# Kernel tuning notes

Hardware: AMD Instinct MI355X
Metric: run time of the kernel (lower is better)

The kernel has to match this reference:

```python
import jax, jax.numpy as jnp
import numpy as np

B, S, E = 2, 2048, 2048
HQ, HKV, D = 16, 4, 128
WINDOW = 512
ROPE_BASE = 10000.0


def apply_rope(x):
    # x: [B, H, S, D]; rotate-half RoPE, positions start at 0 (prefill, no cache)
    half = x.shape[-1] // 2
    inv_freq = 1.0 / (ROPE_BASE ** (jnp.arange(half, dtype=jnp.float32) / half))
    ang = jnp.arange(x.shape[2], dtype=jnp.float32)[:, None] * inv_freq[None, :]  # [S, half]
    cos, sin = jnp.cos(ang), jnp.sin(ang)
    x1, x2 = x[..., :half], x[..., half:]
    return jnp.concatenate([x1 * cos - x2 * sin, x1 * sin + x2 * cos], axis=-1)


def setup_inputs() -> dict:
    key = jax.random.key(0)
    ks = jax.random.split(key, 9)
    sc = 0.02
    return {
        "x": jax.random.normal(ks[0], (B, S, E), dtype=jnp.float32),
        "Wq": jax.random.normal(ks[1], (HQ * D, E), dtype=jnp.float32) * sc,
        "bq": jnp.zeros((HQ * D,), dtype=jnp.float32),
        "Wk": jax.random.normal(ks[2], (HKV * D, E), dtype=jnp.float32) * sc,
        "bk": jnp.zeros((HKV * D,), dtype=jnp.float32),
        "Wv": jax.random.normal(ks[3], (HKV * D, E), dtype=jnp.float32) * sc,
        "bv": jnp.zeros((HKV * D,), dtype=jnp.float32),
        "Wo": jax.random.normal(ks[4], (E, HQ * D), dtype=jnp.float32) * sc,
        "bo": jnp.zeros((E,), dtype=jnp.float32),
    }


def reference(x, Wq, bq, Wk, bk, Wv, bv, Wo, bo):
    b, s, _ = x.shape
    group = HQ // HKV
    # projections (torch Linear: y = x @ W.T + b)
    Q = (x @ Wq.T + bq).reshape(b, s, HQ, D).transpose(0, 2, 1, 3)     # [B,HQ,S,D]
    K = (x @ Wk.T + bk).reshape(b, s, HKV, D).transpose(0, 2, 1, 3)    # [B,HKV,S,D]
    V = (x @ Wv.T + bv).reshape(b, s, HKV, D).transpose(0, 2, 1, 3)
    Q = apply_rope(Q)
    K = apply_rope(K)
    # GQA: group query heads per KV head instead of repeating K/V (same math)
    Qg = Q.reshape(b, HKV, group, s, D)
    scores = jnp.einsum('bkgqd,bkyd->bkgqy', Qg, K) / jnp.sqrt(jnp.float32(D))
    # sliding-window causal mask: j <= i and i - j <= window_size
    i = jnp.arange(s)[:, None]
    j = jnp.arange(s)[None, :]
    allowed = (j <= i) & ((i - j) <= WINDOW)
    scores = jnp.where(allowed, scores, jnp.float32(-jnp.inf))
    w = jax.nn.softmax(scores, axis=-1)
    out = jnp.einsum('bkgqy,bkyd->bkgqd', w, V)                        # [B,HKV,G,S,D]
    out = out.reshape(b, HQ, s, D).transpose(0, 2, 1, 3).reshape(b, s, HQ * D)
    out = out @ Wo.T + bo  # dropout is identity at inference
    return out
```

## Files before the change

kernel.cpp:

```cpp
#include <hip/hip_runtime.h>
#include <hip/hip_bf16.h>

typedef unsigned short u16;
typedef unsigned int u32;
typedef __attribute__((ext_vector_type(4))) unsigned short ushort4_t;
typedef __attribute__((ext_vector_type(8))) short short8;
typedef __attribute__((ext_vector_type(4))) float f32x4;

#define B_ 2
#define S_ 2048
#define E_ 2048
#define HQ_ 16
#define HKV_ 4
#define D_ 128
#define WINDOW_ 512

static __device__ __forceinline__ float bf2f(u16 u) {
    union { unsigned int i; float f; } v; v.i = ((unsigned int)u) << 16; return v.f;
}
static __device__ __forceinline__ u16 f2bf(float f) {
    unsigned int x = __float_as_uint(f);
    unsigned int r = (x + 0x7fffu + ((x >> 16) & 1u)) >> 16;
    return (u16)r;
}

static __device__ __forceinline__ void gload_lds16(const u16* g, u16* l) {
    __builtin_amdgcn_global_load_lds(
        (const __attribute__((address_space(1))) unsigned int*)g,
        (__attribute__((address_space(3))) unsigned int*)l,
        16, 0, 0);
}

static __device__ __forceinline__ int detect_fp32(const u16* wq, int* cnt_sh) {
    if (threadIdx.x == 0) *cnt_sh = 0;
    __syncthreads();
    int c = 0;
    #pragma unroll
    for (int k = 0; k < 4; ++k) {
        u16 v = wq[threadIdx.x * 4 + k];
        if (((v >> 7) & 0xFF) >= 0x90) c++;
    }
    atomicAdd(cnt_sh, c);
    __syncthreads();
    return (*cnt_sh >= 64) ? 1 : 0;
}

#define C_WQ   8388608u
#define C_WK   12582912u
#define C_WV   13631488u
#define C_BQ   14680064u
#define C_BK   14682112u
#define C_BV   14682624u
#define C_WO   14683136u
#define C_BO   18877440u
#define NTOT   18879488u

__global__ __launch_bounds__(256) void convert_kernel(
    const void* p0, const void* p1, const void* p2, const void* p3, const void* p4,
    const void* p5, const void* p6, const void* p7, const void* p8,
    u16* __restrict__ C, int* __restrict__ flagout)
{
    __shared__ int cnt;
    const int f = detect_fp32((const u16*)p1, &cnt);
    if (blockIdx.x == 0 && threadIdx.x == 0) *flagout = f;

    unsigned int idx = (blockIdx.x * 256u + threadIdx.x) * 4u;
    if (idx >= NTOT) return;

    const void* src; unsigned int local;
    if      (idx < C_WQ) { src = p0; local = idx; }
    else if (idx < C_WK) { src = p1; local = idx - C_WQ; }
    else if (idx < C_WV) { src = p3; local = idx - C_WK; }
    else if (idx < C_BQ) { src = p5; local = idx - C_WV; }
    else if (idx < C_BK) { src = p2; local = idx - C_BQ; }
    else if (idx < C_BV) { src = p4; local = idx - C_BK; }
    else if (idx < C_WO) { src = p6; local = idx - C_BV; }
    else if (idx < C_BO) { src = p7; local = idx - C_WO; }
    else                 { src = p8; local = idx - C_BO; }

    ushort4_t o;
    if (f) {
        float4 v = *(const float4*)((const float*)src + local);
        o[0] = f2bf(v.x); o[1] = f2bf(v.y); o[2] = f2bf(v.z); o[3] = f2bf(v.w);
    } else {
        o = *(const ushort4_t*)((const u16*)src + local);
    }
    *(ushort4_t*)(C + idx) = o;
}

#define SCHED __builtin_amdgcn_sched_barrier(0)

__global__ __launch_bounds__(512, 2) void gemm256(
    const u16* __restrict__ A, const u16* __restrict__ W,
    const u16* __restrict__ bias, u16* __restrict__ C,
    int M, int N, int K)
{
    __shared__ __align__(16) u16 lds[65536];

    const int m0 = blockIdx.y * 256, n0 = blockIdx.x * 256;
    const int t = threadIdx.x;
    const int wv = t >> 6, lane = t & 63;
    const int wm = wv >> 2, wn = wv & 3;
    const int quad = lane >> 4, l16 = lane & 15;
    const int h3 = l16 & 7;

    const int rr = t >> 3;
    const int sblk = ((t & 7) ^ (rr & 7)) * 8;

    const u16* Asrc = A + (size_t)(m0 + rr) * K + sblk;
    const u16* Bsrc = W + (size_t)(n0 + rr) * K + sblk;
    u16* ldsA = lds + wv * 512;
    u16* ldsB = lds + 16384 + wv * 512;

#define STAGE_A(slot, Qi, k0) gload_lds16(Asrc + (size_t)((Qi) * 64) * K + (k0), ldsA + (slot) * 32768 + (Qi) * 4096)
#define STAGE_B(slot, Qi, k0) gload_lds16(Bsrc + (size_t)((Qi) * 64) * K + (k0), ldsB + (slot) * 32768 + (Qi) * 4096)

    f32x4 acc[8][4];
    #pragma unroll
    for (int mi = 0; mi < 8; ++mi)
        #pragma unroll
        for (int ni = 0; ni < 4; ++ni)
            acc[mi][ni] = (f32x4){0.f, 0.f, 0.f, 0.f};

    const int NT = K / 64;

    #pragma unroll
    for (int q = 0; q < 4; ++q) STAGE_A(0, q, 0);
    #pragma unroll
    for (int q = 0; q < 4; ++q) STAGE_B(0, q, 0);
    SCHED;
    STAGE_A(1, 0, 64);
    STAGE_A(1, 2, 64);
    SCHED;
    asm volatile("s_waitcnt vmcnt(2)" ::: "memory");
    __builtin_amdgcn_s_barrier();
    SCHED;

    short8 aA[4][2], aB[4][2];
    short8 b0[2][2], b1[2][2];

#define DSREAD_A(dst, qm_)                                                     \
    _Pragma("unroll")                                                          \
    for (int fr = 0; fr < 4; ++fr) {                                           \
        const int r = wm * 128 + (qm_) * 64 + fr * 16 + l16;                   \
        _Pragma("unroll")                                                      \
        for (int kk = 0; kk < 2; ++kk)                                         \
            dst[fr][kk] = *(const short8*)(As + r * 64 + (((kk * 4 + quad) ^ h3) << 3)); \
    }

#define DSREAD_B(dst, qn_)                                                     \
    _Pragma("unroll")                                                          \
    for (int g = 0; g < 2; ++g) {                                              \
        const int r = wn * 64 + (qn_) * 32 + g * 16 + l16;                     \
        _Pragma("unroll")                                                      \
        for (int kk = 0; kk < 2; ++kk)                                         \
            dst[g][kk] = *(const short8*)(Bs + r * 64 + (((kk * 4 + quad) ^ h3) << 3)); \
    }

#define MFMA_PH(qm_, afrag, bfrag, qn_)                                        \
    __builtin_amdgcn_s_setprio(1);                                             \
    _Pragma("unroll")                                                          \
    for (int g = 0; g < 2; ++g)                                                \
        _Pragma("unroll")                                                      \
        for (int fr = 0; fr < 4; ++fr)                                         \
            _Pragma("unroll")                                                  \
            for (int kk = 0; kk < 2; ++kk)                                     \
                acc[(qm_) * 4 + fr][(qn_) * 2 + g] =                           \
                    __builtin_amdgcn_mfma_f32_16x16x32_bf16(                   \
                        afrag[fr][kk], bfrag[g][kk], acc[(qm_) * 4 + fr][(qn_) * 2 + g], 0, 0, 0); \
    __builtin_amdgcn_s_setprio(0);

#define BAR_LGKM                                                               \
    __builtin_amdgcn_s_barrier();                                              \
    asm volatile("s_waitcnt lgkmcnt(0)" ::: "memory");                         \
    SCHED;

#define BAR_TRAIL                                                              \
    SCHED;                                                                     \
    __builtin_amdgcn_s_barrier();                                              \
    SCHED;

    for (int kt = 0; kt < NT; ++kt) {
        const int slot = kt & 1;
        const u16* As = lds + slot * 32768;
        const u16* Bs = As + 16384;

        const int kB = (kt + 1) * 64;
        const int kA = (kt + 2) * 64;
        const int sB = slot ^ 1;
        const bool doE = (kt <= NT - 2);
        const bool doM = (kt <= NT - 3);

        DSREAD_A(aA, 0);
        DSREAD_B(b0, 0);
        SCHED;
        if (doE) { STAGE_A(sB, 1, kB); STAGE_A(sB, 3, kB); }
        SCHED;
        BAR_LGKM;
        MFMA_PH(0, aA, b0, 0);
        BAR_TRAIL;

        DSREAD_B(b1, 1);
        SCHED;
        if (doE) { STAGE_B(sB, 0, kB); STAGE_B(sB, 1, kB); }
        SCHED;
        BAR_LGKM;
        MFMA_PH(0, aA, b1, 1);
        BAR_TRAIL;

        DSREAD_A(aB, 1);
        SCHED;
        if (doE) { STAGE_B(sB, 2, kB); STAGE_B(sB, 3, kB); }
        SCHED;
        BAR_LGKM;
        MFMA_PH(1, aB, b1, 1);
        BAR_TRAIL;

        if (doM) { STAGE_A(slot, 0, kA); STAGE_A(slot, 2, kA); }
        SCHED;
        if (kt == NT - 2)     asm volatile("s_waitcnt vmcnt(0)" ::: "memory");
        else if (kt < NT - 2) asm volatile("s_waitcnt vmcnt(2)" ::: "memory");
        SCHED;
        __builtin_amdgcn_s_barrier();
        SCHED;
        MFMA_PH(1, aB, b0, 0);
        BAR_TRAIL;
    }

#undef STAGE_A
#undef STAGE_B
#undef DSREAD_A
#undef DSREAD_B
#undef MFMA_PH

    #pragma unroll
    for (int mi = 0; mi < 8; ++mi) {
        #pragma unroll
        for (int ni = 0; ni < 4; ++ni) {
            const int row0 = m0 + wm * 128 + mi * 16 + quad * 4;
            const int col  = n0 + wn * 64 + ni * 16 + l16;
            const float bb = bf2f(bias[col]);
            #pragma unroll
            for (int r = 0; r < 4; ++r)
                C[(size_t)(row0 + r) * N + col] = f2bf(acc[mi][ni][r] + bb);
        }
    }
}

__global__ __launch_bounds__(512, 2) void gemm_out_p(
    const u16* __restrict__ A, const u16* __restrict__ W,
    const u16* __restrict__ bias, void* __restrict__ Cout,
    int M, int N, int K, const int* __restrict__ flagp)
{
    __shared__ __align__(16) u16 lds[49152];

    const int m0 = blockIdx.y * 128, n0 = blockIdx.x * 256;
    const int t = threadIdx.x;
    const int wv = t >> 6, lane = t & 63;
    const int wm = wv >> 2, wn = wv & 3;
    const int quad = lane >> 4, l16 = lane & 15;
    const int h3 = l16 & 7;

    const int rr = t >> 3;
    const int sblk = ((t & 7) ^ (rr & 7)) * 8;

    const u16* Asrc = A + (size_t)(m0 + rr) * K + sblk;
    const u16* Bsrc = W + (size_t)(n0 + rr) * K + sblk;
    u16* ldsA = lds + wv * 512;
    u16* ldsB = lds + 8192 + wv * 512;

#define STAGE_A(slot, Qi, k0) gload_lds16(Asrc + (size_t)((Qi) * 64) * K + (k0), ldsA + (slot) * 24576 + (Qi) * 4096)
#define STAGE_B(slot, Qi, k0) gload_lds16(Bsrc + (size_t)((Qi) * 64) * K + (k0), ldsB + (slot) * 24576 + (Qi) * 4096)

    f32x4 acc[4][4];
    #pragma unroll
    for (int mi = 0; mi < 4; ++mi)
        #pragma unroll
        for (int ni = 0; ni < 4; ++ni)
            acc[mi][ni] = (f32x4){0.f, 0.f, 0.f, 0.f};

    const int NT = K / 64;

    STAGE_A(0, 0, 0); STAGE_A(0, 1, 0);
    STAGE_B(0, 0, 0); STAGE_B(0, 1, 0); STAGE_B(0, 2, 0); STAGE_B(0, 3, 0);
    SCHED;
    STAGE_A(1, 0, 64);
    SCHED;
    asm volatile("s_waitcnt vmcnt(1)" ::: "memory");
    __builtin_amdgcn_s_barrier();
    SCHED;

    short8 aA[4][2];
    short8 b0[2][2], b1[2][2];

#define DSREAD_A(dst)                                                          \
    _Pragma("unroll")                                                          \
    for (int fr = 0; fr < 4; ++fr) {                                           \
        const int r = wm * 64 + fr * 16 + l16;                                 \
        _Pragma("unroll")                                                      \
        for (int kk = 0; kk < 2; ++kk)                                         \
            dst[fr][kk] = *(const short8*)(As + r * 64 + (((kk * 4 + quad) ^ h3) << 3)); \
    }

#define DSREAD_B(dst, qn_)                                                     \
    _Pragma("unroll")                                                          \
    for (int g = 0; g < 2; ++g) {                                              \
        const int r = wn * 64 + (qn_) * 32 + g * 16 + l16;                     \
        _Pragma("unroll")                                                      \
        for (int kk = 0; kk < 2; ++kk)                                         \
            dst[g][kk] = *(const short8*)(Bs + r * 64 + (((kk * 4 + quad) ^ h3) << 3)); \
    }

#define MFMA_PH(bfrag, qn_)                                                    \
    __builtin_amdgcn_s_setprio(1);                                             \
    _Pragma("unroll")                                                          \
    for (int g = 0; g < 2; ++g)                                                \
        _Pragma("unroll")                                                      \
        for (int fr = 0; fr < 4; ++fr)                                         \
            _Pragma("unroll")                                                  \
            for (int kk = 0; kk < 2; ++kk)                                     \
                acc[fr][(qn_) * 2 + g] =                                       \
                    __builtin_amdgcn_mfma_f32_16x16x32_bf16(                   \
                        aA[fr][kk], bfrag[g][kk], acc[fr][(qn_) * 2 + g], 0, 0, 0); \
    __builtin_amdgcn_s_setprio(0);

    for (int kt = 0; kt < NT; ++kt) {
        const int slot = kt & 1;
        const u16* As = lds + slot * 24576;
        const u16* Bs = As + 8192;

        const int kB = (kt + 1) * 64;
        const int kA = (kt + 2) * 64;
        const int sB = slot ^ 1;
        const bool doE = (kt <= NT - 2);
        const bool doM = (kt <= NT - 3);

        DSREAD_A(aA);
        DSREAD_B(b0, 0);
        SCHED;
        if (doE) { STAGE_A(sB, 1, kB); STAGE_B(sB, 0, kB); STAGE_B(sB, 1, kB); }
        SCHED;
        __builtin_amdgcn_s_barrier();
        asm volatile("s_waitcnt lgkmcnt(0)" ::: "memory");
        SCHED;
        MFMA_PH(b0, 0);
        SCHED;
        __builtin_amdgcn_s_barrier();
        SCHED;

        DSREAD_B(b1, 1);
        SCHED;
        if (doE) { STAGE_B(sB, 2, kB); STAGE_B(sB, 3, kB); }
        if (doM) { STAGE_A(slot, 0, kA); }
        SCHED;
        if (kt == NT - 2)     asm volatile("s_waitcnt vmcnt(0)" ::: "memory");
        else if (kt < NT - 2) asm volatile("s_waitcnt vmcnt(1)" ::: "memory");
        SCHED;
        __builtin_amdgcn_s_barrier();
        asm volatile("s_waitcnt lgkmcnt(0)" ::: "memory");
        SCHED;
        MFMA_PH(b1, 1);
        SCHED;
        __builtin_amdgcn_s_barrier();
        SCHED;
    }

#undef STAGE_A
#undef STAGE_B
#undef DSREAD_A
#undef DSREAD_B
#undef MFMA_PH

    const int f = *flagp;
    #pragma unroll
    for (int mi = 0; mi < 4; ++mi) {
        #pragma unroll
        for (int ni = 0; ni < 4; ++ni) {
            const int row0 = m0 + wm * 64 + mi * 16 + quad * 4;
            const int col  = n0 + wn * 64 + ni * 16 + l16;
            const float bb = bf2f(bias[col]);
            #pragma unroll
            for (int r = 0; r < 4; ++r) {
                float val = acc[mi][ni][r] + bb;
                size_t idx = (size_t)(row0 + r) * N + col;
                if (f) ((float*)Cout)[idx] = val;
                else   ((u16*)Cout)[idx]   = f2bf(val);
            }
        }
    }
}

#define ROPE_BLOCKS 20480

__global__ __launch_bounds__(256) void rope_transpose(
    u16* __restrict__ QKV, u16* __restrict__ VT)
{
    if (blockIdx.x < ROPE_BLOCKS) {
        const size_t qtot = (size_t)B_ * S_ * HQ_ * 64;
        size_t idx = (size_t)blockIdx.x * 256 + threadIdx.x;

        int d; size_t tok; u16* p;
        if (idx < qtot) {
            d = (int)(idx & 63);
            size_t th = idx >> 6;
            int h = (int)(th & 15);
            tok = th >> 4;
            p = QKV + tok * 3072 + h * 128 + d;
        } else {
            size_t r = idx - qtot;
            d = (int)(r & 63);
            size_t th = r >> 6;
            int kh = (int)(th & 3);
            tok = th >> 2;
            p = QKV + tok * 3072 + 2048 + kh * 128 + d;
        }
        int s = (int)(tok & (S_ - 1));

        float x1 = bf2f(p[0]);
        float x2 = bf2f(p[64]);
        float inv_freq = __expf(-0.14391156514f * (float)d);
        float ang = (float)s * inv_freq;
        float sn, cs;
        __sincosf(ang, &sn, &cs);
        p[0]  = f2bf(x1 * cs - x2 * sn);
        p[64] = f2bf(x1 * sn + x2 * cs);
    } else {
        const int bid = blockIdx.x - ROPE_BLOCKS;
        const int t = threadIdx.x;
        const int s_blk = bid & 63;
        const int dh = (bid >> 6) & 1;
        const int bkh = bid >> 7;
        const int b = bkh >> 2, kh = bkh & 3;

        const int d = dh * 64 + (t & 63);
        const int s0 = s_blk * 32 + (t >> 6) * 8;

        const u16* src = QKV + (size_t)(b * S_ + s0) * 3072 + 2560 + kh * 128 + d;
        short8 v;
        #pragma unroll
        for (int j = 0; j < 8; ++j)
            v[j] = (short)src[(size_t)j * 3072];
        *(short8*)(VT + ((size_t)(bkh * 128 + d)) * S_ + s0) = v;
    }
}

__global__ __launch_bounds__(256) void attn_mfma(
    const u16* __restrict__ QKV, const u16* __restrict__ VT, u16* __restrict__ O)
{
    __shared__ __align__(16) u16 Ks[32 * 136];
    __shared__ __align__(16) u16 Vs[128 * 40];
    __shared__ __align__(16) u16 ps[4][16 * 40];

    const int t = threadIdx.x;
    const int wv = t >> 6, lane = t & 63;
    const int quad = lane >> 4, l16 = lane & 15;

    const int h = blockIdx.x & 15;
    const int tile = (blockIdx.x >> 4) & 31;
    const int b = blockIdx.x >> 9;
    const int kh = h >> 2;

    const int i0b = tile * 64;
    const int i0w = i0b + wv * 16;
    const float scale = 0.08838834764831845f;
    const float CEXP = 8.0f;

    short8 qf[4];
    {
        const u16* qrow = QKV + (size_t)(b * S_ + i0w + l16) * 3072 + h * 128 + quad * 8;
        #pragma unroll
        for (int kc = 0; kc < 4; ++kc)
            qf[kc] = *(const short8*)(qrow + kc * 32);
    }

    short8 ones;
    #pragma unroll
    for (int j = 0; j < 8; ++j) ones[j] = (short)0x3F80;

    f32x4 oc[8];
    #pragma unroll
    for (int c = 0; c < 8; ++c) oc[c] = (f32x4){0.f, 0.f, 0.f, 0.f};
    f32x4 ocl = (f32x4){0.f, 0.f, 0.f, 0.f};

    int jlo = i0b - WINDOW_; if (jlo < 0) jlo = 0;
    const int nblk = (i0b + 64 - jlo) >> 5;

    const u16* VTb = VT + (size_t)(b * 4 + kh) * 128 * S_;

    for (int blk = 0; blk < nblk; ++blk) {
        const int jbase = jlo + blk * 32;
        __syncthreads();
        #pragma unroll
        for (int it = 0; it < 2; ++it) {
            int idx = it * 256 + t;
            int key = idx >> 4;
            int c8  = (idx & 15) * 8;
            int row = ((key & 1) << 4) | (key >> 1);
            short8 kvv = *(const short8*)(QKV + (size_t)(b * S_ + jbase + key) * 3072 + 2048 + kh * 128 + c8);
            *(short8*)(Ks + row * 136 + c8) = kvv;
        }
        #pragma unroll
        for (int it = 0; it < 2; ++it) {
            int idx = it * 256 + t;
            int d = idx >> 2;
            int q4 = idx & 3;
            short8 vvv = *(const short8*)(VTb + (size_t)d * S_ + jbase + q4 * 8);
            *(short8*)(Vs + d * 40 + q4 * 8) = vvv;
        }
        __syncthreads();

        bool active = (jbase <= i0w + 15) && (jbase + 31 >= i0w - WINDOW_);
        if (!active) continue;

        f32x4 sc0 = {0.f,0.f,0.f,0.f}, sc1 = {0.f,0.f,0.f,0.f};
        #pragma unroll
        for (int kc = 0; kc < 4; ++kc) {
            short8 kb0 = *(const short8*)(Ks + l16 * 136 + kc * 32 + quad * 8);
            short8 kb1 = *(const short8*)(Ks + (16 + l16) * 136 + kc * 32 + quad * 8);
            sc0 = __builtin_amdgcn_mfma_f32_16x16x32_bf16(qf[kc], kb0, sc0, 0, 0, 0);
            sc1 = __builtin_amdgcn_mfma_f32_16x16x32_bf16(qf[kc], kb1, sc1, 0, 0, 0);
        }

        const int j0 = jbase + 2 * l16;
        const int iq = i0w + quad * 4;
        u16* pw = ps[wv];
        #pragma unroll
        for (int r = 0; r < 4; ++r) {
            int i = iq + r;
            bool ok0 = (unsigned)(i - j0)     <= (unsigned)WINDOW_;
            bool ok1 = (unsigned)(i - j0 - 1) <= (unsigned)WINDOW_;
            float p0 = ok0 ? __expf(sc0[r] * scale - CEXP) : 0.f;
            float p1 = ok1 ? __expf(sc1[r] * scale - CEXP) : 0.f;
            u32 pk = ((u32)f2bf(p1) << 16) | (u32)f2bf(p0);
            *(u32*)(pw + (quad * 4 + r) * 40 + 2 * l16) = pk;
        }
        short8 pa = *(const short8*)(pw + l16 * 40 + quad * 8);

        #pragma unroll
        for (int c = 0; c < 8; ++c) {
            short8 vb = *(const short8*)(Vs + (c * 16 + l16) * 40 + quad * 8);
            oc[c] = __builtin_amdgcn_mfma_f32_16x16x32_bf16(pa, vb, oc[c], 0, 0, 0);
        }
        ocl = __builtin_amdgcn_mfma_f32_16x16x32_bf16(pa, ones, ocl, 0, 0, 0);
    }

    float inv0[4];
    #pragma unroll
    for (int r = 0; r < 4; ++r) inv0[r] = 1.0f / ocl[r];
    #pragma unroll
    for (int c = 0; c < 8; ++c) {
        #pragma unroll
        for (int r = 0; r < 4; ++r) {
            O[((size_t)(b * S_ + i0w + quad * 4 + r) * HQ_ + h) * D_ + c * 16 + l16] =
                f2bf(oc[c][r] * inv0[r]);
        }
    }
}

extern "C" void kernel_launch(void* const* d_in, const int* in_sizes, int n_in,
                              void* d_out, int out_size, void* d_ws, size_t ws_size,
                              hipStream_t stream)
{
    char* ws = (char*)d_ws;
    u16* Cc   = (u16*)ws;
    int* flag = (int*)(ws + 37758976);
    u16* QKV  = (u16*)(ws + 37759232);
    u16* Ab   = (u16*)(ws + 37759232 + 25165824);

    const u16* xb    = Cc;
    u16*       VT    = Cc;
    const u16* Wqkv  = Cc + C_WQ;
    const u16* bqkv  = Cc + C_BQ;
    const u16* Wob   = Cc + C_WO;
    const u16* bob   = Cc + C_BO;

    const int M = B_ * S_;
    dim3 blk(256);

    convert_kernel<<<dim3(NTOT / 4 / 256), blk, 0, stream>>>(
        d_in[0], d_in[1], d_in[2], d_in[3], d_in[4], d_in[5], d_in[6], d_in[7], d_in[8],
        Cc, flag);

    gemm256<<<dim3(3072 / 256, M / 256), dim3(512), 0, stream>>>(
        xb, Wqkv, bqkv, QKV, M, 3072, E_);

    rope_transpose<<<dim3(ROPE_BLOCKS + 1024), blk, 0, stream>>>(QKV, VT);

    attn_mfma<<<dim3(B_ * HQ_ * (S_ / 64)), blk, 0, stream>>>(QKV, VT, Ab);

    gemm_out_p<<<dim3(E_ / 256, M / 128), dim3(512), 0, stream>>>(
        Ab, Wob, bob, d_out, M, E_, HQ_ * D_, flag);
}
```

Baseline: 316.6 us.

## Restructure GEMM main loops to prefetch next A fragments and cut barriers

Both GEMM kernels (QKV projection and output projection) get a new software pipeline. All B fragments for the current tile are read from LDS up front, and the next tile's A fragments are read from the other LDS slot after a single barrier. Several per-phase barriers are replaced with partial lgkmcnt waits, and the second kernel alternates two A register sets with a two-step unroll. The goal is less barrier and LDS-latency stall between MFMA phases. In exchange it uses more registers and waits on vmcnt(0) every iteration, so global prefetch depth drops.

```diff
diff --git a/kernel.cpp b/kernel.cpp
--- a/kernel.cpp
+++ b/kernel.cpp
@@ -124,10 +124,9 @@
 
     const int NT = K / 64;
 
-    #pragma unroll
-    for (int q = 0; q < 4; ++q) STAGE_A(0, q, 0);
-    #pragma unroll
-    for (int q = 0; q < 4; ++q) STAGE_B(0, q, 0);
+    STAGE_A(0, 0, 0); STAGE_A(0, 2, 0);
+    STAGE_B(0, 0, 0); STAGE_B(0, 1, 0); STAGE_B(0, 2, 0); STAGE_B(0, 3, 0);
+    STAGE_A(0, 1, 0); STAGE_A(0, 3, 0);
     SCHED;
     STAGE_A(1, 0, 64);
     STAGE_A(1, 2, 64);
@@ -139,22 +138,22 @@
     short8 aA[4][2], aB[4][2];
     short8 b0[2][2], b1[2][2];
 
-#define DSREAD_A(dst, qm_)                                                     \
+#define DSREAD_A(dst, qm_, base)                                               \
     _Pragma("unroll")                                                          \
     for (int fr = 0; fr < 4; ++fr) {                                           \
         const int r = wm * 128 + (qm_) * 64 + fr * 16 + l16;                   \
         _Pragma("unroll")                                                      \
         for (int kk = 0; kk < 2; ++kk)                                         \
-            dst[fr][kk] = *(const short8*)(As + r * 64 + (((kk * 4 + quad) ^ h3) << 3)); \
-    }
-
-#define DSREAD_B(dst, qn_)                                                     \
+            dst[fr][kk] = *(const short8*)((base) + r * 64 + (((kk * 4 + quad) ^ h3) << 3)); \
+    }
+
+#define DSREAD_B(dst, qn_, base)                                               \
     _Pragma("unroll")                                                          \
     for (int g = 0; g < 2; ++g) {                                              \
         const int r = wn * 64 + (qn_) * 32 + g * 16 + l16;                     \
         _Pragma("unroll")                                                      \
         for (int kk = 0; kk < 2; ++kk)                                         \
-            dst[g][kk] = *(const short8*)(Bs + r * 64 + (((kk * 4 + quad) ^ h3) << 3)); \
+            dst[g][kk] = *(const short8*)((base) + r * 64 + (((kk * 4 + quad) ^ h3) << 3)); \
     }
 
 #define MFMA_PH(qm_, afrag, bfrag, qn_)                                        \
@@ -170,20 +169,14 @@
                         afrag[fr][kk], bfrag[g][kk], acc[(qm_) * 4 + fr][(qn_) * 2 + g], 0, 0, 0); \
     __builtin_amdgcn_s_setprio(0);
 
-#define BAR_LGKM                                                               \
-    __builtin_amdgcn_s_barrier();                                              \
-    asm volatile("s_waitcnt lgkmcnt(0)" ::: "memory");                         \
-    SCHED;
-
-#define BAR_TRAIL                                                              \
-    SCHED;                                                                     \
-    __builtin_amdgcn_s_barrier();                                              \
+    DSREAD_A(aA, 0, lds);
     SCHED;
 
     for (int kt = 0; kt < NT; ++kt) {
         const int slot = kt & 1;
         const u16* As = lds + slot * 32768;
         const u16* Bs = As + 16384;
+        const u16* AsN = lds + (slot ^ 1) * 32768;
 
         const int kB = (kt + 1) * 64;
         const int kA = (kt + 2) * 64;
@@ -191,40 +184,38 @@
         const bool doE = (kt <= NT - 2);
         const bool doM = (kt <= NT - 3);
 
-        DSREAD_A(aA, 0);
-        DSREAD_B(b0, 0);
-        SCHED;
-        if (doE) { STAGE_A(sB, 1, kB); STAGE_A(sB, 3, kB); }
-        SCHED;
-        BAR_LGKM;
+        DSREAD_B(b0, 0, Bs);
+        DSREAD_B(b1, 1, Bs);
+        DSREAD_A(aB, 1, As);
+        SCHED;
+        if (doE) { STAGE_B(sB, 0, kB); STAGE_B(sB, 1, kB);
+                   STAGE_B(sB, 2, kB); STAGE_B(sB, 3, kB);
+                   STAGE_A(sB, 1, kB); STAGE_A(sB, 3, kB); }
+        SCHED;
+
+        asm volatile("s_waitcnt lgkmcnt(12)" ::: "memory");
+        SCHED;
         MFMA_PH(0, aA, b0, 0);
-        BAR_TRAIL;
-
-        DSREAD_B(b1, 1);
-        SCHED;
-        if (doE) { STAGE_B(sB, 0, kB); STAGE_B(sB, 1, kB); }
-        SCHED;
-        BAR_LGKM;
+        SCHED;
+        asm volatile("s_waitcnt lgkmcnt(8)" ::: "memory");
+        SCHED;
         MFMA_PH(0, aA, b1, 1);
-        BAR_TRAIL;
-
-        DSREAD_A(aB, 1);
-        SCHED;
-        if (doE) { STAGE_B(sB, 2, kB); STAGE_B(sB, 3, kB); }
-        SCHED;
-        BAR_LGKM;
+        SCHED;
+        asm volatile("s_waitcnt lgkmcnt(0)" ::: "memory");
+        SCHED;
+        if (doE) asm volatile("s_waitcnt vmcnt(0)" ::: "memory");
+        SCHED;
+        __builtin_amdgcn_s_barrier();
+        SCHED;
+
+        if (doM) { STAGE_A(slot, 0, kA); STAGE_A(slot, 2, kA); }
+        SCHED;
+        if (doE) { DSREAD_A(aA, 0, AsN); }
+        SCHED;
         MFMA_PH(1, aB, b1, 1);
-        BAR_TRAIL;
-
-        if (doM) { STAGE_A(slot, 0, kA); STAGE_A(slot, 2, kA); }
-        SCHED;
-        if (kt == NT - 2)     asm volatile("s_waitcnt vmcnt(0)" ::: "memory");
-        else if (kt < NT - 2) asm volatile("s_waitcnt vmcnt(2)" ::: "memory");
-        SCHED;
-        __builtin_amdgcn_s_barrier();
         SCHED;
         MFMA_PH(1, aB, b0, 0);
-        BAR_TRAIL;
+        SCHED;
     }
 
 #undef STAGE_A
@@ -284,34 +275,32 @@
     STAGE_A(0, 0, 0); STAGE_A(0, 1, 0);
     STAGE_B(0, 0, 0); STAGE_B(0, 1, 0); STAGE_B(0, 2, 0); STAGE_B(0, 3, 0);
     SCHED;
-    STAGE_A(1, 0, 64);
-    SCHED;
-    asm volatile("s_waitcnt vmcnt(1)" ::: "memory");
+    asm volatile("s_waitcnt vmcnt(0)" ::: "memory");
     __builtin_amdgcn_s_barrier();
     SCHED;
 
-    short8 aA[4][2];
+    short8 aAe[4][2], aAo[4][2];
     short8 b0[2][2], b1[2][2];
 
-#define DSREAD_A(dst)                                                          \
+#define DSREAD_A2(dst, base)                                                   \
     _Pragma("unroll")                                                          \
     for (int fr = 0; fr < 4; ++fr) {                                           \
         const int r = wm * 64 + fr * 16 + l16;                                 \
         _Pragma("unroll")                                                      \
         for (int kk = 0; kk < 2; ++kk)                                         \
-            dst[fr][kk] = *(const short8*)(As + r * 64 + (((kk * 4 + quad) ^ h3) << 3)); \
-    }
-
-#define DSREAD_B(dst, qn_)                                                     \
+            dst[fr][kk] = *(const short8*)((base) + r * 64 + (((kk * 4 + quad) ^ h3) << 3)); \
+    }
+
+#define DSREAD_B2(dst, qn_, base)                                              \
     _Pragma("unroll")                                                          \
     for (int g = 0; g < 2; ++g) {                                              \
         const int r = wn * 64 + (qn_) * 32 + g * 16 + l16;                     \
         _Pragma("unroll")                                                      \
         for (int kk = 0; kk < 2; ++kk)                                         \
-            dst[g][kk] = *(const short8*)(Bs + r * 64 + (((kk * 4 + quad) ^ h3) << 3)); \
-    }
-
-#define MFMA_PH(bfrag, qn_)                                                    \
+            dst[g][kk] = *(const short8*)((base) + r * 64 + (((kk * 4 + quad) ^ h3) << 3)); \
+    }
+
+#define MFMA_PH2(afrag, bfrag, qn_)                                            \
     __builtin_amdgcn_s_setprio(1);                                             \
     _Pragma("unroll")                                                          \
     for (int g = 0; g < 2; ++g)                                                \
@@ -321,55 +310,56 @@
             for (int kk = 0; kk < 2; ++kk)                                     \
                 acc[fr][(qn_) * 2 + g] =                                       \
                     __builtin_amdgcn_mfma_f32_16x16x32_bf16(                   \
-                        aA[fr][kk], bfrag[g][kk], acc[fr][(qn_) * 2 + g], 0, 0, 0); \
+                        afrag[fr][kk], bfrag[g][kk], acc[fr][(qn_) * 2 + g], 0, 0, 0); \
     __builtin_amdgcn_s_setprio(0);
 
-    for (int kt = 0; kt < NT; ++kt) {
-        const int slot = kt & 1;
-        const u16* As = lds + slot * 24576;
-        const u16* Bs = As + 8192;
-
-        const int kB = (kt + 1) * 64;
-        const int kA = (kt + 2) * 64;
-        const int sB = slot ^ 1;
-        const bool doE = (kt <= NT - 2);
-        const bool doM = (kt <= NT - 3);
-
-        DSREAD_A(aA);
-        DSREAD_B(b0, 0);
-        SCHED;
-        if (doE) { STAGE_A(sB, 1, kB); STAGE_B(sB, 0, kB); STAGE_B(sB, 1, kB); }
-        SCHED;
-        __builtin_amdgcn_s_barrier();
-        asm volatile("s_waitcnt lgkmcnt(0)" ::: "memory");
-        SCHED;
-        MFMA_PH(b0, 0);
-        SCHED;
-        __builtin_amdgcn_s_barrier();
-        SCHED;
-
-        DSREAD_B(b1, 1);
-        SCHED;
-        if (doE) { STAGE_B(sB, 2, kB); STAGE_B(sB, 3, kB); }
-        if (doM) { STAGE_A(slot, 0, kA); }
-        SCHED;
-        if (kt == NT - 2)     asm volatile("s_waitcnt vmcnt(0)" ::: "memory");
-        else if (kt < NT - 2) asm volatile("s_waitcnt vmcnt(1)" ::: "memory");
-        SCHED;
-        __builtin_amdgcn_s_barrier();
-        asm volatile("s_waitcnt lgkmcnt(0)" ::: "memory");
-        SCHED;
-        MFMA_PH(b1, 1);
-        SCHED;
-        __builtin_amdgcn_s_barrier();
-        SCHED;
+#define TILE_OUT(kt_, AAc, AAn)                                                \
+    {                                                                          \
+        const int slot = (kt_) & 1;                                            \
+        const u16* As = lds + slot * 24576;                                    \
+        const u16* Bs = As + 8192;                                             \
+        const u16* AsN = lds + (slot ^ 1) * 24576;                             \
+        const int kB = ((kt_) + 1) * 64;                                       \
+        const int sB = slot ^ 1;                                               \
+        const bool doE = ((kt_) <= NT - 2);                                    \
+        (void)As;                                                              \
+        DSREAD_B2(b0, 0, Bs);                                                  \
+        DSREAD_B2(b1, 1, Bs);                                                  \
+        SCHED;                                                                 \
+        if (doE) { STAGE_A(sB, 0, kB); STAGE_A(sB, 1, kB);                     \
+                   STAGE_B(sB, 0, kB); STAGE_B(sB, 1, kB);                     \
+                   STAGE_B(sB, 2, kB); STAGE_B(sB, 3, kB); }                   \
+        SCHED;                                                                 \
+        asm volatile("s_waitcnt lgkmcnt(4)" ::: "memory");                     \
+        SCHED;                                                                 \
+        MFMA_PH2(AAc, b0, 0);                                                  \
+        SCHED;                                                                 \
+        asm volatile("s_waitcnt lgkmcnt(0)" ::: "memory");                     \
+        SCHED;                                                                 \
+        if (doE) asm volatile("s_waitcnt vmcnt(0)" ::: "memory");              \
+        SCHED;                                                                 \
+        __builtin_amdgcn_s_barrier();                                          \
+        SCHED;                                                                 \
+        if (doE) { DSREAD_A2(AAn, AsN); }                                      \
+        SCHED;                                                                 \
+        MFMA_PH2(AAc, b1, 1);                                                  \
+        SCHED;                                                                 \
+    }
+
+    DSREAD_A2(aAe, lds);
+    SCHED;
+
+    for (int kt = 0; kt < NT; kt += 2) {
+        TILE_OUT(kt,     aAe, aAo);
+        TILE_OUT(kt + 1, aAo, aAe);
     }
 
 #undef STAGE_A
 #undef STAGE_B
-#undef DSREAD_A
-#undef DSREAD_B
-#undef MFMA_PH
+#undef DSREAD_A2
+#undef DSREAD_B2
+#undef MFMA_PH2
+#undef TILE_OUT
 
     const int f = *flagp;
     #pragma unroll
```

New measurement: 308.4 us. 2.6% less time.

## Cut barriers in GEMM pipelines and process two KV blocks per attention sync

Applied to the files above, without the earlier changes.

Both GEMM main loops are restructured: the wait-and-barrier moves to the top of each k-step, LDS fragment reads are issued earlier, and all next-tile global-to-LDS stages are issued together. The per-phase barriers are replaced by partial lgkmcnt waits and one barrier per iteration. The aim is to cut barrier stalls and let MFMA overlap LDS and global traffic. The attention kernel now loads 64 keys (two 32-key K/V buffers) per __syncthreads pair, halving block syncs at the cost of more LDS. The fewer barriers and new waitcnt counts risk races if the counts are wrong.

```diff
diff --git a/kernel.cpp b/kernel.cpp
--- a/kernel.cpp
+++ b/kernel.cpp
@@ -131,9 +131,6 @@
     SCHED;
     STAGE_A(1, 0, 64);
     STAGE_A(1, 2, 64);
-    SCHED;
-    asm volatile("s_waitcnt vmcnt(2)" ::: "memory");
-    __builtin_amdgcn_s_barrier();
     SCHED;
 
     short8 aA[4][2], aB[4][2];
@@ -170,61 +167,56 @@
                         afrag[fr][kk], bfrag[g][kk], acc[(qm_) * 4 + fr][(qn_) * 2 + g], 0, 0, 0); \
     __builtin_amdgcn_s_setprio(0);
 
-#define BAR_LGKM                                                               \
-    __builtin_amdgcn_s_barrier();                                              \
-    asm volatile("s_waitcnt lgkmcnt(0)" ::: "memory");                         \
-    SCHED;
-
-#define BAR_TRAIL                                                              \
-    SCHED;                                                                     \
-    __builtin_amdgcn_s_barrier();                                              \
-    SCHED;
-
     for (int kt = 0; kt < NT; ++kt) {
         const int slot = kt & 1;
         const u16* As = lds + slot * 32768;
         const u16* Bs = As + 16384;
 
+        if (kt == NT - 1) asm volatile("s_waitcnt vmcnt(0)" ::: "memory");
+        else              asm volatile("s_waitcnt vmcnt(2)" ::: "memory");
+        __builtin_amdgcn_s_barrier();
+        SCHED;
+
         const int kB = (kt + 1) * 64;
         const int kA = (kt + 2) * 64;
         const int sB = slot ^ 1;
-        const bool doE = (kt <= NT - 2);
-        const bool doM = (kt <= NT - 3);
+        const bool doEarly = (kt <= NT - 2);
+        const bool doMid   = (kt <= NT - 3);
 
         DSREAD_A(aA, 0);
         DSREAD_B(b0, 0);
         SCHED;
-        if (doE) { STAGE_A(sB, 1, kB); STAGE_A(sB, 3, kB); }
-        SCHED;
-        BAR_LGKM;
+        DSREAD_B(b1, 1);
+        SCHED;
+
+        if (doEarly) { STAGE_A(sB, 1, kB); STAGE_A(sB, 3, kB);
+                       STAGE_B(sB, 0, kB); STAGE_B(sB, 1, kB);
+                       STAGE_B(sB, 2, kB); STAGE_B(sB, 3, kB); }
+        SCHED;
+
+        asm volatile("s_waitcnt lgkmcnt(4)" ::: "memory");
+        SCHED;
+        DSREAD_A(aB, 1);
+        SCHED;
+
         MFMA_PH(0, aA, b0, 0);
-        BAR_TRAIL;
-
-        DSREAD_B(b1, 1);
-        SCHED;
-        if (doE) { STAGE_B(sB, 0, kB); STAGE_B(sB, 1, kB); }
-        SCHED;
-        BAR_LGKM;
+        SCHED;
+        asm volatile("s_waitcnt lgkmcnt(8)" ::: "memory");
+        SCHED;
         MFMA_PH(0, aA, b1, 1);
-        BAR_TRAIL;
-
-        DSREAD_A(aB, 1);
-        SCHED;
-        if (doE) { STAGE_B(sB, 2, kB); STAGE_B(sB, 3, kB); }
-        SCHED;
-        BAR_LGKM;
+        SCHED;
+        asm volatile("s_waitcnt lgkmcnt(0)" ::: "memory");
+        SCHED;
+        __builtin_amdgcn_s_barrier();
+        SCHED;
+
+        if (doMid) { STAGE_A(slot, 0, kA); STAGE_A(slot, 2, kA); }
+        SCHED;
+
         MFMA_PH(1, aB, b1, 1);
-        BAR_TRAIL;
-
-        if (doM) { STAGE_A(slot, 0, kA); STAGE_A(slot, 2, kA); }
-        SCHED;
-        if (kt == NT - 2)     asm volatile("s_waitcnt vmcnt(0)" ::: "memory");
-        else if (kt < NT - 2) asm volatile("s_waitcnt vmcnt(2)" ::: "memory");
-        SCHED;
-        __builtin_amdgcn_s_barrier();
         SCHED;
         MFMA_PH(1, aB, b0, 0);
-        BAR_TRAIL;
+        SCHED;
     }
 
 #undef STAGE_A
@@ -285,9 +277,6 @@
     STAGE_B(0, 0, 0); STAGE_B(0, 1, 0); STAGE_B(0, 2, 0); STAGE_B(0, 3, 0);
     SCHED;
     STAGE_A(1, 0, 64);
-    SCHED;
-    asm volatile("s_waitcnt vmcnt(1)" ::: "memory");
-    __builtin_amdgcn_s_barrier();
     SCHED;
 
     short8 aA[4][2];
@@ -329,39 +318,42 @@
         const u16* As = lds + slot * 24576;
         const u16* Bs = As + 8192;
 
+        if (kt == NT - 1) asm volatile("s_waitcnt vmcnt(0)" ::: "memory");
+        else              asm volatile("s_waitcnt vmcnt(1)" ::: "memory");
+        __builtin_amdgcn_s_barrier();
+        SCHED;
+
         const int kB = (kt + 1) * 64;
         const int kA = (kt + 2) * 64;
         const int sB = slot ^ 1;
-        const bool doE = (kt <= NT - 2);
-        const bool doM = (kt <= NT - 3);
+        const bool doEarly = (kt <= NT - 2);
+        const bool doMid   = (kt <= NT - 3);
 
         DSREAD_A(aA);
         DSREAD_B(b0, 0);
         SCHED;
-        if (doE) { STAGE_A(sB, 1, kB); STAGE_B(sB, 0, kB); STAGE_B(sB, 1, kB); }
+        DSREAD_B(b1, 1);
+        SCHED;
+
+        if (doEarly) { STAGE_A(sB, 1, kB);
+                       STAGE_B(sB, 0, kB); STAGE_B(sB, 1, kB);
+                       STAGE_B(sB, 2, kB); STAGE_B(sB, 3, kB); }
+        SCHED;
+
+        asm volatile("s_waitcnt lgkmcnt(4)" ::: "memory");
+        SCHED;
+
+        MFMA_PH(b0, 0);
+        SCHED;
+        asm volatile("s_waitcnt lgkmcnt(0)" ::: "memory");
         SCHED;
         __builtin_amdgcn_s_barrier();
-        asm volatile("s_waitcnt lgkmcnt(0)" ::: "memory");
-        SCHED;
-        MFMA_PH(b0, 0);
-        SCHED;
-        __builtin_amdgcn_s_barrier();
-        SCHED;
-
-        DSREAD_B(b1, 1);
-        SCHED;
-        if (doE) { STAGE_B(sB, 2, kB); STAGE_B(sB, 3, kB); }
-        if (doM) { STAGE_A(slot, 0, kA); }
-        SCHED;
-        if (kt == NT - 2)     asm volatile("s_waitcnt vmcnt(0)" ::: "memory");
-        else if (kt < NT - 2) asm volatile("s_waitcnt vmcnt(1)" ::: "memory");
-        SCHED;
-        __builtin_amdgcn_s_barrier();
-        asm volatile("s_waitcnt lgkmcnt(0)" ::: "memory");
-        SCHED;
+        SCHED;
+
+        if (doMid) { STAGE_A(slot, 0, kA); }
+        SCHED;
+
         MFMA_PH(b1, 1);
-        SCHED;
-        __builtin_amdgcn_s_barrier();
         SCHED;
     }
 
@@ -447,8 +439,8 @@
 __global__ __launch_bounds__(256) void attn_mfma(
     const u16* __restrict__ QKV, const u16* __restrict__ VT, u16* __restrict__ O)
 {
-    __shared__ __align__(16) u16 Ks[32 * 136];
-    __shared__ __align__(16) u16 Vs[128 * 40];
+    __shared__ __align__(16) u16 Ks[2][32 * 136];
+    __shared__ __align__(16) u16 Vs[2][128 * 40];
     __shared__ __align__(16) u16 ps[4][16 * 40];
 
     const int t = threadIdx.x;
@@ -483,65 +475,73 @@
     f32x4 ocl = (f32x4){0.f, 0.f, 0.f, 0.f};
 
     int jlo = i0b - WINDOW_; if (jlo < 0) jlo = 0;
-    const int nblk = (i0b + 64 - jlo) >> 5;
+    const int npair = (i0b + 64 - jlo) >> 6;
 
     const u16* VTb = VT + (size_t)(b * 4 + kh) * 128 * S_;
 
-    for (int blk = 0; blk < nblk; ++blk) {
-        const int jbase = jlo + blk * 32;
+    for (int pp = 0; pp < npair; ++pp) {
+        const int jb0 = jlo + pp * 64;
         __syncthreads();
         #pragma unroll
-        for (int it = 0; it < 2; ++it) {
-            int idx = it * 256 + t;
-            int key = idx >> 4;
-            int c8  = (idx & 15) * 8;
-            int row = ((key & 1) << 4) | (key >> 1);
-            short8 kvv = *(const short8*)(QKV + (size_t)(b * S_ + jbase + key) * 3072 + 2048 + kh * 128 + c8);
-            *(short8*)(Ks + row * 136 + c8) = kvv;
-        }
-        #pragma unroll
-        for (int it = 0; it < 2; ++it) {
-            int idx = it * 256 + t;
-            int d = idx >> 2;
-            int q4 = idx & 3;
-            short8 vvv = *(const short8*)(VTb + (size_t)d * S_ + jbase + q4 * 8);
-            *(short8*)(Vs + d * 40 + q4 * 8) = vvv;
+        for (int c = 0; c < 2; ++c) {
+            const int jb = jb0 + c * 32;
+            #pragma unroll
+            for (int it = 0; it < 2; ++it) {
+                int idx = it * 256 + t;
+                int key = idx >> 4;
+                int c8  = (idx & 15) * 8;
+                int row = ((key & 1) << 4) | (key >> 1);
+                short8 kvv = *(const short8*)(QKV + (size_t)(b * S_ + jb + key) * 3072 + 2048 + kh * 128 + c8);
+                *(short8*)(Ks[c] + row * 136 + c8) = kvv;
+            }
+            #pragma unroll
+            for (int it = 0; it < 2; ++it) {
+                int idx = it * 256 + t;
+                int d = idx >> 2;
+                int q4 = idx & 3;
+                short8 vvv = *(const short8*)(VTb + (size_t)d * S_ + jb + q4 * 8);
+                *(short8*)(Vs[c] + d * 40 + q4 * 8) = vvv;
+            }
         }
         __syncthreads();
 
-        bool active = (jbase <= i0w + 15) && (jbase + 31 >= i0w - WINDOW_);
-        if (!active) continue;
-
-        f32x4 sc0 = {0.f,0.f,0.f,0.f}, sc1 = {0.f,0.f,0.f,0.f};
-        #pragma unroll
-        for (int kc = 0; kc < 4; ++kc) {
-            short8 kb0 = *(const short8*)(Ks + l16 * 136 + kc * 32 + quad * 8);
-            short8 kb1 = *(const short8*)(Ks + (16 + l16) * 136 + kc * 32 + quad * 8);
-            sc0 = __builtin_amdgcn_mfma_f32_16x16x32_bf16(qf[kc], kb0, sc0, 0, 0, 0);
-            sc1 = __builtin_amdgcn_mfma_f32_16x16x32_bf16(qf[kc], kb1, sc1, 0, 0, 0);
+        #pragma unroll
+        for (int c = 0; c < 2; ++c) {
+            const int jbase = jb0 + c * 32;
+            bool active = (jbase <= i0w + 15) && (jbase + 31 >= i0w - WINDOW_);
+            if (!active) continue;
+
+            f32x4 sc0 = {0.f,0.f,0.f,0.f}, sc1 = {0.f,0.f,0.f,0.f};
+            #pragma unroll
+            for (int kc = 0; kc < 4; ++kc) {
+                short8 kb0 = *(const short8*)(Ks[c] + l16 * 136 + kc * 32 + quad * 8);
+                short8 kb1 = *(const short8*)(Ks[c] + (16 + l16) * 136 + kc * 32 + quad * 8);
+                sc0 = __builtin_amdgcn_mfma_f32_16x16x32_bf16(qf[kc], kb0, sc0, 0, 0, 0);
+                sc1 = __builtin_amdgcn_mfma_f32_16x16x32_bf16(qf[kc], kb1, sc1, 0, 0, 0);
+            }
+
+            const int j0 = jbase + 2 * l16;
+            const int iq = i0w + quad * 4;
+            u16* pw = ps[wv];
+            #pragma unroll
+            for (int r = 0; r < 4; ++r) {
+                int i = iq + r;
+                bool ok0 = (unsigned)(i - j0)     <= (unsigned)WINDOW_;
+                bool ok1 = (unsigned)(i - j0 - 1) <= (unsigned)WINDOW_;
+                float p0 = ok0 ? __expf(sc0[r] * scale - CEXP) : 0.f;
+                float p1 = ok1 ? __expf(sc1[r] * scale - CEXP) : 0.f;
+                u32 pk = ((u32)f2bf(p1) << 16) | (u32)f2bf(p0);
+                *(u32*)(pw + (quad * 4 + r) * 40 + 2 * l16) = pk;
+            }
+            short8 pa = *(const short8*)(pw + l16 * 40 + quad * 8);
+
+            #pragma unroll
+            for (int cc = 0; cc < 8; ++cc) {
+                short8 vb = *(const short8*)(Vs[c] + (cc * 16 + l16) * 40 + quad * 8);
+                oc[cc] = __builtin_amdgcn_mfma_f32_16x16x32_bf16(pa, vb, oc[cc], 0, 0, 0);
+            }
+            ocl = __builtin_amdgcn_mfma_f32_16x16x32_bf16(pa, ones, ocl, 0, 0, 0);
         }
-
-        const int j0 = jbase + 2 * l16;
-        const int iq = i0w + quad * 4;
-        u16* pw = ps[wv];
-        #pragma unroll
-        for (int r = 0; r < 4; ++r) {
-            int i = iq + r;
-            bool ok0 = (unsigned)(i - j0)     <= (unsigned)WINDOW_;
-            bool ok1 = (unsigned)(i - j0 - 1) <= (unsigned)WINDOW_;
-            float p0 = ok0 ? __expf(sc0[r] * scale - CEXP) : 0.f;
-            float p1 = ok1 ? __expf(sc1[r] * scale - CEXP) : 0.f;
-            u32 pk = ((u32)f2bf(p1) << 16) | (u32)f2bf(p0);
-            *(u32*)(pw + (quad * 4 + r) * 40 + 2 * l16) = pk;
-        }
-        short8 pa = *(const short8*)(pw + l16 * 40 + quad * 8);
-
-        #pragma unroll
-        for (int c = 0; c < 8; ++c) {
-            short8 vb = *(const short8*)(Vs + (c * 16 + l16) * 40 + quad * 8);
-            oc[c] = __builtin_amdgcn_mfma_f32_16x16x32_bf16(pa, vb, oc[c], 0, 0, 0);
-        }
-        ocl = __builtin_amdgcn_mfma_f32_16x16x32_bf16(pa, ones, ocl, 0, 0, 0);
     }
 
     float inv0[4];
```

New measurement: 291.7 us. 7.9% less time.
